# Optimization experiments

Measured on AMD Instinct MI355X. Metric: run time of the kernel, lower is better.

Reference implementation:

```python
import jax, jax.numpy as jnp
import numpy as np

MARGIN = 1.0


def _pairwise_sq_dist(emb):
    # squared euclidean distances, clamped at 0, diagonal zeroed (as in torch ref)
    ab = emb @ emb.T
    sq = jnp.diag(ab)
    d = jnp.maximum(sq[:, None] - 2.0 * ab + sq[None, :], 0.0)
    d = d * (d > 0.0).astype(d.dtype)  # error_mask step (faithful)
    B = d.shape[0]
    return d * (1.0 - jnp.eye(B, dtype=d.dtype))


def setup_inputs() -> dict:
    key = jax.random.key(0)
    k1, k2 = jax.random.split(key)
    emb = jax.random.normal(k1, (512, 256), dtype=jnp.float32)
    labels = jax.random.randint(k2, (512,), 0, 64, dtype=jnp.int64)
    return {"input": emb, "target": labels}


def reference(input, target):
    emb = input.astype(jnp.float32)
    pd = _pairwise_sq_dist(emb)                      # [B, B]
    B = pd.shape[0]
    adj = target[:, None] == target[None, :]         # [B, B]
    adj_not = ~adj

    # mask3[j, i, k]: negative k valid for anchor j w/ positive i (semi-hard: d(j,k) > d(j,i))
    mask3 = adj_not[:, None, :] & (pd[:, None, :] > pd[:, :, None])  # [B, B, B]

    # masked min over k: min of valid negatives, rowmax where masked out (torch trick equivalent)
    rowmax = pd.max(axis=1)                          # [B]
    negatives_outside = jnp.min(
        jnp.where(mask3, pd[:, None, :], rowmax[:, None, None]), axis=2
    )                                                # [B(anchor j), B(pos i)]

    # fallback: largest negative distance per anchor (masked max, rowmin where masked out)
    rowmin = pd.min(axis=1)                          # [B]
    negatives_inside = jnp.max(
        jnp.where(adj_not, pd, rowmin[:, None]), axis=1
    )                                                # [B]

    mask_final = jnp.any(mask3, axis=2)              # [B, B]
    semi_hard = jnp.where(mask_final, negatives_outside, negatives_inside[:, None])

    loss_mat = MARGIN + pd - semi_hard
    mask_pos = adj.astype(jnp.float32) - jnp.eye(B, dtype=jnp.float32)
    num_pos = mask_pos.sum()
    loss = jnp.maximum(loss_mat * mask_pos, 0.0).sum() / num_pos
    return loss.astype(input.dtype)
```

## Files before the change

### kernel.cpp

```cpp
#include <hip/hip_runtime.h>


__device__ inline float wave_max(float v){
  #pragma unroll
  for (int o = 32; o > 0; o >>= 1) v = fmaxf(v, __shfl_xor(v, o));
  return v;
}
__device__ inline float wave_min(float v){
  #pragma unroll
  for (int o = 32; o > 0; o >>= 1) v = fminf(v, __shfl_xor(v, o));
  return v;
}
__device__ inline float wave_sum(float v){
  #pragma unroll
  for (int o = 32; o > 0; o >>= 1) v += __shfl_xor(v, o);
  return v;
}

__global__ __launch_bounds__(256) void triplet_main(
    const float* __restrict__ emb, const int* __restrict__ labels,
    float* __restrict__ pl, float* __restrict__ pc)
{
  __shared__ float4 tile[32][65];
  __shared__ float part[8][96];
  __shared__ float pdrow[2][512];
  __shared__ float sqarr[512];
  __shared__ int   lab[512];
  __shared__ int   plist[2][512];
  __shared__ int   pcount[2];
  __shared__ float redm[4][4];
  __shared__ float scal[2];

  const int t   = threadIdx.x;
  const int ja0 = blockIdx.x * 2, ja1 = ja0 + 1;
  const int kl  = t & 31;
  const int q   = t >> 5;
  const int lane = t & 63, wid = t >> 6;
  const float4* embf4 = reinterpret_cast<const float4*>(emb);

  lab[t]       = labels[t];
  lab[t + 256] = labels[t + 256];
  if (t < 2) pcount[t] = 0;

  float4 ej0[8], ej1[8];
  #pragma unroll
  for (int i = 0; i < 8; ++i){
    ej0[i] = embf4[ja0 * 64 + q * 8 + i];
    ej1[i] = embf4[ja1 * 64 + q * 8 + i];
  }

  for (int ti = 0; ti < 16; ++ti){
    __syncthreads();
    const int kbase = ti * 32;
    #pragma unroll
    for (int j = 0; j < 8; ++j){
      int idx = t + j * 256;
      int r = idx >> 6, c = idx & 63;
      tile[r][c] = embf4[(kbase + r) * 64 + c];
    }
    __syncthreads();
    float a0 = 0.f, a1 = 0.f, as = 0.f;
    #pragma unroll
    for (int i = 0; i < 8; ++i){
      float4 e = tile[kl][q * 8 + i];
      float4 x = ej0[i], y = ej1[i];
      a0 += e.x*x.x + e.y*x.y + e.z*x.z + e.w*x.w;
      a1 += e.x*y.x + e.y*y.y + e.z*y.z + e.w*y.w;
      as += e.x*e.x + e.y*e.y + e.z*e.z + e.w*e.w;
    }
    part[q][kl]      = a0;
    part[q][32 + kl] = a1;
    part[q][64 + kl] = as;
    __syncthreads();
    if (t < 96){
      int qty = t >> 5, k2 = t & 31;
      float s = 0.f;
      #pragma unroll
      for (int qq = 0; qq < 8; ++qq) s += part[qq][qty * 32 + k2];
      int kg = kbase + k2;
      if (qty == 0)      pdrow[0][kg] = s;
      else if (qty == 1) pdrow[1][kg] = s;
      else               sqarr[kg]    = s;
    }
  }
  __syncthreads();

  const float sq0 = sqarr[ja0], sq1 = sqarr[ja1];
  #pragma unroll
  for (int j = 0; j < 2; ++j){
    int k = t + j * 256;
    float sk = sqarr[k];
    float d0 = fmaxf(sq0 - 2.f * pdrow[0][k] + sk, 0.f);
    float d1 = fmaxf(sq1 - 2.f * pdrow[1][k] + sk, 0.f);
    pdrow[0][k] = (k == ja0) ? 0.f : d0;
    pdrow[1][k] = (k == ja1) ? 0.f : d1;
  }
  __syncthreads();

  const int lj0 = lab[ja0], lj1 = lab[ja1];
  float ni0 = 0.f, ni1 = 0.f;
  #pragma unroll
  for (int j = 0; j < 2; ++j){
    int k = t + j * 256;
    float p0 = pdrow[0][k], p1 = pdrow[1][k];
    int lk = lab[k];
    if (lk != lj0) ni0 = fmaxf(ni0, p0);
    if (lk != lj1) ni1 = fmaxf(ni1, p1);
    if (k != ja0 && lk == lj0) plist[0][atomicAdd(&pcount[0], 1)] = k;
    if (k != ja1 && lk == lj1) plist[1][atomicAdd(&pcount[1], 1)] = k;
  }
  ni0 = wave_max(ni0); ni1 = wave_max(ni1);
  if (lane == 0){ redm[wid][0] = ni0; redm[wid][1] = ni1; }
  __syncthreads();
  if (t == 0){
    scal[0] = fmaxf(fmaxf(redm[0][0], redm[1][0]), fmaxf(redm[2][0], redm[3][0]));
    scal[1] = fmaxf(fmaxf(redm[0][1], redm[1][1]), fmaxf(redm[2][1], redm[3][1]));
  }
  __syncthreads();

  float wacc = 0.f;
  #pragma unroll 1
  for (int a = 0; a < 2; ++a){
    const int   P       = pcount[a];
    const int   lj      = a ? lj1 : lj0;
    const float ninside = scal[a];
    const float* pda    = pdrow[a];
    for (int p = wid; p < P; p += 4){
      int   i   = plist[a][p];
      float tiv = pda[i];
      float vmin = 3.402823466e38f;
      #pragma unroll
      for (int m = 0; m < 8; ++m){
        int k = lane + m * 64;
        float pk = pda[k];
        if (lab[k] != lj && pk > tiv) vmin = fminf(vmin, pk);
      }
      vmin = wave_min(vmin);
      float semi = (vmin < 3.0e38f) ? vmin : ninside;
      float c = fmaxf(1.0f + tiv - semi, 0.0f);
      if (lane == 0) wacc += c;
    }
  }
  wacc = wave_sum(wacc);
  if (lane == 0) redm[wid][2] = wacc;
  __syncthreads();
  if (t == 0){
    pl[blockIdx.x] = redm[0][2] + redm[1][2] + redm[2][2] + redm[3][2];
    pc[blockIdx.x] = (float)(pcount[0] + pcount[1]);
  }
}

__global__ __launch_bounds__(256) void triplet_final(
    const float* __restrict__ pl, const float* __restrict__ pc,
    float* __restrict__ out)
{
  int t = threadIdx.x;
  float s = pl[t];
  float c = pc[t];
  s = wave_sum(s);
  c = wave_sum(c);
  __shared__ float rs[4], rc[4];
  int wid = t >> 6, lane = t & 63;
  if (lane == 0){ rs[wid] = s; rc[wid] = c; }
  __syncthreads();
  if (t == 0)
    out[0] = (rs[0] + rs[1] + rs[2] + rs[3]) / (rc[0] + rc[1] + rc[2] + rc[3]);
}

extern "C" void kernel_launch(void* const* d_in, const int* in_sizes, int n_in,
                              void* d_out, int out_size, void* d_ws, size_t ws_size,
                              hipStream_t stream) {
  const float* emb    = (const float*)d_in[0];
  const int*   labels = (const int*)d_in[1];
  float* out = (float*)d_out;
  float* pl  = (float*)d_ws;
  float* pc  = pl + 256;
  triplet_main<<<256, 256, 0, stream>>>(emb, labels, pl, pc);
  triplet_final<<<1, 256, 0, stream>>>(pl, pc, out);
}
```

Before: 78.53 us.

## Split into tiled distance GEMM kernel and per-row wave-level mining kernel

Replaces the fused per-anchor-pair kernel, which recomputed a full 512-row dot product sweep per block, with a 32x32 tiled GEMM that writes the full distance matrix to workspace. A second kernel assigns one wave per anchor row, holds the row in registers, and enumerates positives with ballots instead of shared-memory lists and atomics. The final reduction now uses global atomics plus a last-block ticket, which removes the separate finalize kernel. The cost is a 1 MB round trip through global memory, and the ticket counter depends on the GEMM kernel zeroing it first.

```diff
diff --git a/kernel.cpp b/kernel.cpp
--- a/kernel.cpp
+++ b/kernel.cpp
@@ -1,170 +1,153 @@
 #include <hip/hip_runtime.h>
 
 
-__device__ inline float wave_max(float v){
+#define BN 512
+#define DF4 64
+
+__device__ inline float wave_max64(float v){
   #pragma unroll
   for (int o = 32; o > 0; o >>= 1) v = fmaxf(v, __shfl_xor(v, o));
   return v;
 }
-__device__ inline float wave_min(float v){
+__device__ inline float wave_min64(float v){
   #pragma unroll
   for (int o = 32; o > 0; o >>= 1) v = fminf(v, __shfl_xor(v, o));
   return v;
 }
-__device__ inline float wave_sum(float v){
+
+__global__ __launch_bounds__(256) void pd_gemm(
+    const float* __restrict__ emb, float* __restrict__ pd, float* __restrict__ acc)
+{
+  __shared__ float As[32][260];
+  __shared__ float Bs[32][260];
+  __shared__ float sqA[32], sqB[32];
+  __shared__ float outt[32][36];
+
+  const int t  = threadIdx.x;
+  const int bi = blockIdx.x & 15, bj = blockIdx.x >> 4;
+  const int R0 = bi * 32, C0 = bj * 32;
+  const float4* ef4 = reinterpret_cast<const float4*>(emb);
+
+  if (blockIdx.x == 0 && t == 0){ acc[0] = 0.f; acc[1] = 0.f; ((int*)acc)[2] = 0; }
+
   #pragma unroll
-  for (int o = 32; o > 0; o >>= 1) v += __shfl_xor(v, o);
-  return v;
-}
-
-__global__ __launch_bounds__(256) void triplet_main(
-    const float* __restrict__ emb, const int* __restrict__ labels,
-    float* __restrict__ pl, float* __restrict__ pc)
-{
-  __shared__ float4 tile[32][65];
-  __shared__ float part[8][96];
-  __shared__ float pdrow[2][512];
-  __shared__ float sqarr[512];
-  __shared__ int   lab[512];
-  __shared__ int   plist[2][512];
-  __shared__ int   pcount[2];
-  __shared__ float redm[4][4];
-  __shared__ float scal[2];
-
-  const int t   = threadIdx.x;
-  const int ja0 = blockIdx.x * 2, ja1 = ja0 + 1;
-  const int kl  = t & 31;
-  const int q   = t >> 5;
-  const int lane = t & 63, wid = t >> 6;
-  const float4* embf4 = reinterpret_cast<const float4*>(emb);
-
-  lab[t]       = labels[t];
-  lab[t + 256] = labels[t + 256];
-  if (t < 2) pcount[t] = 0;
-
-  float4 ej0[8], ej1[8];
-  #pragma unroll
-  for (int i = 0; i < 8; ++i){
-    ej0[i] = embf4[ja0 * 64 + q * 8 + i];
-    ej1[i] = embf4[ja1 * 64 + q * 8 + i];
+  for (int j = 0; j < 8; ++j){
+    int idx = t + j * 256;
+    int r = idx >> 6, c = idx & 63;
+    float4 va = ef4[(R0 + r) * DF4 + c];
+    float4 vb = ef4[(C0 + r) * DF4 + c];
+    *(float4*)&As[r][c * 4] = va;
+    *(float4*)&Bs[r][c * 4] = vb;
   }
-
-  for (int ti = 0; ti < 16; ++ti){
-    __syncthreads();
-    const int kbase = ti * 32;
+  {
+    int half = t >> 7, u = t & 127;
+    int r = u >> 2, part = u & 3;
+    int base = ((half ? C0 : R0) + r) * DF4 + part * 16;
+    float s = 0.f;
     #pragma unroll
-    for (int j = 0; j < 8; ++j){
-      int idx = t + j * 256;
-      int r = idx >> 6, c = idx & 63;
-      tile[r][c] = embf4[(kbase + r) * 64 + c];
+    for (int i = 0; i < 16; ++i){
+      float4 v = ef4[base + i];
+      s += v.x*v.x + v.y*v.y + v.z*v.z + v.w*v.w;
     }
-    __syncthreads();
-    float a0 = 0.f, a1 = 0.f, as = 0.f;
-    #pragma unroll
-    for (int i = 0; i < 8; ++i){
-      float4 e = tile[kl][q * 8 + i];
-      float4 x = ej0[i], y = ej1[i];
-      a0 += e.x*x.x + e.y*x.y + e.z*x.z + e.w*x.w;
-      a1 += e.x*y.x + e.y*y.y + e.z*y.z + e.w*y.w;
-      as += e.x*e.x + e.y*e.y + e.z*e.z + e.w*e.w;
-    }
-    part[q][kl]      = a0;
-    part[q][32 + kl] = a1;
-    part[q][64 + kl] = as;
-    __syncthreads();
-    if (t < 96){
-      int qty = t >> 5, k2 = t & 31;
-      float s = 0.f;
-      #pragma unroll
-      for (int qq = 0; qq < 8; ++qq) s += part[qq][qty * 32 + k2];
-      int kg = kbase + k2;
-      if (qty == 0)      pdrow[0][kg] = s;
-      else if (qty == 1) pdrow[1][kg] = s;
-      else               sqarr[kg]    = s;
-    }
+    s += __shfl_xor(s, 1); s += __shfl_xor(s, 2);
+    if (part == 0){ if (half) sqB[r] = s; else sqA[r] = s; }
   }
   __syncthreads();
 
-  const float sq0 = sqarr[ja0], sq1 = sqarr[ja1];
-  #pragma unroll
-  for (int j = 0; j < 2; ++j){
-    int k = t + j * 256;
-    float sk = sqarr[k];
-    float d0 = fmaxf(sq0 - 2.f * pdrow[0][k] + sk, 0.f);
-    float d1 = fmaxf(sq1 - 2.f * pdrow[1][k] + sk, 0.f);
-    pdrow[0][k] = (k == ja0) ? 0.f : d0;
-    pdrow[1][k] = (k == ja1) ? 0.f : d1;
+  const int r0 = t & 15, r1 = r0 + 16;
+  const int c0 = t >> 4, c1 = c0 + 16;
+  float a00 = 0.f, a01 = 0.f, a10 = 0.f, a11 = 0.f;
+  #pragma unroll 8
+  for (int kg = 0; kg < 64; ++kg){
+    float4 A0 = *(const float4*)&As[r0][kg * 4];
+    float4 A1 = *(const float4*)&As[r1][kg * 4];
+    float4 B0 = *(const float4*)&Bs[c0][kg * 4];
+    float4 B1 = *(const float4*)&Bs[c1][kg * 4];
+    a00 += A0.x*B0.x + A0.y*B0.y + A0.z*B0.z + A0.w*B0.w;
+    a01 += A0.x*B1.x + A0.y*B1.y + A0.z*B1.z + A0.w*B1.w;
+    a10 += A1.x*B0.x + A1.y*B0.y + A1.z*B0.z + A1.w*B0.w;
+    a11 += A1.x*B1.x + A1.y*B1.y + A1.z*B1.z + A1.w*B1.w;
   }
+
+  const float sr0 = sqA[r0], sr1 = sqA[r1];
+  const float sc0 = sqB[c0], sc1 = sqB[c1];
+  float p00 = fmaxf(sr0 + sc0 - 2.f * a00, 0.f);
+  float p01 = fmaxf(sr0 + sc1 - 2.f * a01, 0.f);
+  float p10 = fmaxf(sr1 + sc0 - 2.f * a10, 0.f);
+  float p11 = fmaxf(sr1 + sc1 - 2.f * a11, 0.f);
+  if (bi == bj){
+    if (r0 == c0) p00 = 0.f;
+    if (r0 == c1) p01 = 0.f;
+    if (r1 == c0) p10 = 0.f;
+    if (r1 == c1) p11 = 0.f;
+  }
+  outt[r0][c0] = p00; outt[r0][c1] = p01;
+  outt[r1][c0] = p10; outt[r1][c1] = p11;
   __syncthreads();
 
-  const int lj0 = lab[ja0], lj1 = lab[ja1];
-  float ni0 = 0.f, ni1 = 0.f;
+  int rr = t >> 3, cc = t & 7;
+  float4 v = *(float4*)&outt[rr][cc * 4];
+  *(float4*)&pd[(R0 + rr) * BN + C0 + cc * 4] = v;
+}
+
+__global__ __launch_bounds__(256) void mining(
+    const float* __restrict__ pd, const int* __restrict__ labels,
+    float* __restrict__ acc, float* __restrict__ out)
+{
+  __shared__ float wls[4], wcs[4];
+  const int t = threadIdx.x, lane = t & 63, wid = t >> 6;
+  const int j  = blockIdx.x * 4 + wid;
+  const int lj = labels[j];
+
+  const float4* prow = reinterpret_cast<const float4*>(pd + (size_t)j * BN);
+  const int4*   lrow = reinterpret_cast<const int4*>(labels);
+  float4 p0 = prow[lane * 2], p1 = prow[lane * 2 + 1];
+  int4   l0 = lrow[lane * 2], l1 = lrow[lane * 2 + 1];
+  float pk[8] = {p0.x, p0.y, p0.z, p0.w, p1.x, p1.y, p1.z, p1.w};
+  int   lk[8] = {l0.x, l0.y, l0.z, l0.w, l1.x, l1.y, l1.z, l1.w};
+  const int kbase = lane * 8;
+
+  float ninside = 0.f;
   #pragma unroll
-  for (int j = 0; j < 2; ++j){
-    int k = t + j * 256;
-    float p0 = pdrow[0][k], p1 = pdrow[1][k];
-    int lk = lab[k];
-    if (lk != lj0) ni0 = fmaxf(ni0, p0);
-    if (lk != lj1) ni1 = fmaxf(ni1, p1);
-    if (k != ja0 && lk == lj0) plist[0][atomicAdd(&pcount[0], 1)] = k;
-    if (k != ja1 && lk == lj1) plist[1][atomicAdd(&pcount[1], 1)] = k;
+  for (int m = 0; m < 8; ++m)
+    if (lk[m] != lj) ninside = fmaxf(ninside, pk[m]);
+  ninside = wave_max64(ninside);
+
+  float lsum = 0.f; int pcnt = 0;
+  #pragma unroll
+  for (int m = 0; m < 8; ++m){
+    unsigned long long bal = __ballot(lk[m] == lj && (kbase + m) != j);
+    while (bal){
+      int L = (int)__ffsll((unsigned long long)bal) - 1;
+      bal &= bal - 1;
+      float tiv = __shfl(pk[m], L);
+      float vmin = 3.402823466e38f;
+      #pragma unroll
+      for (int mm = 0; mm < 8; ++mm)
+        if (lk[mm] != lj && pk[mm] > tiv) vmin = fminf(vmin, pk[mm]);
+      vmin = wave_min64(vmin);
+      float semi = (vmin < 3.0e38f) ? vmin : ninside;
+      lsum += fmaxf(1.0f + tiv - semi, 0.f);
+      ++pcnt;
+    }
   }
-  ni0 = wave_max(ni0); ni1 = wave_max(ni1);
-  if (lane == 0){ redm[wid][0] = ni0; redm[wid][1] = ni1; }
+
+  if (lane == 0){ wls[wid] = lsum; wcs[wid] = (float)pcnt; }
   __syncthreads();
   if (t == 0){
-    scal[0] = fmaxf(fmaxf(redm[0][0], redm[1][0]), fmaxf(redm[2][0], redm[3][0]));
-    scal[1] = fmaxf(fmaxf(redm[0][1], redm[1][1]), fmaxf(redm[2][1], redm[3][1]));
-  }
-  __syncthreads();
-
-  float wacc = 0.f;
-  #pragma unroll 1
-  for (int a = 0; a < 2; ++a){
-    const int   P       = pcount[a];
-    const int   lj      = a ? lj1 : lj0;
-    const float ninside = scal[a];
-    const float* pda    = pdrow[a];
-    for (int p = wid; p < P; p += 4){
-      int   i   = plist[a][p];
-      float tiv = pda[i];
-      float vmin = 3.402823466e38f;
-      #pragma unroll
-      for (int m = 0; m < 8; ++m){
-        int k = lane + m * 64;
-        float pk = pda[k];
-        if (lab[k] != lj && pk > tiv) vmin = fminf(vmin, pk);
-      }
-      vmin = wave_min(vmin);
-      float semi = (vmin < 3.0e38f) ? vmin : ninside;
-      float c = fmaxf(1.0f + tiv - semi, 0.0f);
-      if (lane == 0) wacc += c;
+    float bl = wls[0] + wls[1] + wls[2] + wls[3];
+    float bc = wcs[0] + wcs[1] + wcs[2] + wcs[3];
+    atomicAdd(&acc[0], bl);
+    atomicAdd(&acc[1], bc);
+    __threadfence();
+    int tk = atomicAdd((int*)acc + 2, 1);
+    if (tk == 127){
+      __threadfence();
+      float tot = atomicAdd(&acc[0], 0.f);
+      float cnt = atomicAdd(&acc[1], 0.f);
+      out[0] = tot / cnt;
     }
   }
-  wacc = wave_sum(wacc);
-  if (lane == 0) redm[wid][2] = wacc;
-  __syncthreads();
-  if (t == 0){
-    pl[blockIdx.x] = redm[0][2] + redm[1][2] + redm[2][2] + redm[3][2];
-    pc[blockIdx.x] = (float)(pcount[0] + pcount[1]);
-  }
-}
-
-__global__ __launch_bounds__(256) void triplet_final(
-    const float* __restrict__ pl, const float* __restrict__ pc,
-    float* __restrict__ out)
-{
-  int t = threadIdx.x;
-  float s = pl[t];
-  float c = pc[t];
-  s = wave_sum(s);
-  c = wave_sum(c);
-  __shared__ float rs[4], rc[4];
-  int wid = t >> 6, lane = t & 63;
-  if (lane == 0){ rs[wid] = s; rc[wid] = c; }
-  __syncthreads();
-  if (t == 0)
-    out[0] = (rs[0] + rs[1] + rs[2] + rs[3]) / (rc[0] + rc[1] + rc[2] + rc[3]);
 }
 
 extern "C" void kernel_launch(void* const* d_in, const int* in_sizes, int n_in,
@@ -173,8 +156,8 @@
   const float* emb    = (const float*)d_in[0];
   const int*   labels = (const int*)d_in[1];
   float* out = (float*)d_out;
-  float* pl  = (float*)d_ws;
-  float* pc  = pl + 256;
-  triplet_main<<<256, 256, 0, stream>>>(emb, labels, pl, pc);
-  triplet_final<<<1, 256, 0, stream>>>(pl, pc, out);
+  float* pdw = (float*)d_ws;
+  float* acc = pdw + BN * BN;
+  pd_gemm<<<256, 256, 0, stream>>>(emb, pdw, acc);
+  mining<<<128, 256, 0, stream>>>(pdw, labels, acc, out);
 }
```

New measurement: 71.53 us. 8.9% less time.
